# Performance work log

Hardware: AMD Instinct MI355X
Metric: run time of the kernel (lower is better)

The kernel has to match this reference:

```python
import jax, jax.numpy as jnp
import numpy as np

N_BINS = 15  # matches ECELoss(n_bins=15)


def setup_inputs() -> dict:
    key = jax.random.key(0)
    k1, k2 = jax.random.split(key)
    B, C = 2_097_152, 16
    logits = jax.random.normal(k1, (B, C), dtype=jnp.float32) * 2.0
    # binary multi-label targets, stored as float (forward casts to float anyway)
    targets = (jax.random.uniform(k2, (B, C)) < 0.5).astype(jnp.float32)
    return {"logits": logits, "targets": targets}


def reference(logits, targets):
    """Vectorized ECE: single bucketize + segment-sum pass replacing the
    per-class/per-bin Python loops. Same math: for each non-empty (class, bin)
    cell, accumulate |mean_conf - mean_acc| * (cell_count / B), then divide by
    the number of non-empty cells."""
    B, C = logits.shape
    probs = jax.nn.sigmoid(logits)  # [B, C]
    boundaries = jnp.linspace(0.0, 1.0, N_BINS + 1)
    # bin b satisfies boundaries[b] <= p < boundaries[b+1]  (>= start, < end)
    bin_idx = jnp.searchsorted(boundaries, probs, side="right") - 1  # [B, C]
    valid = (bin_idx >= 0) & (bin_idx < N_BINS)  # p == 1.0 falls in no bin
    seg = jnp.where(valid, jnp.arange(C)[None, :] * N_BINS + bin_idx, C * N_BINS)
    seg = seg.reshape(-1)
    num_seg = C * N_BINS + 1  # last segment = dumping ground for invalid
    ones = jnp.ones((B * C,), dtype=probs.dtype)
    cnt = jax.ops.segment_sum(ones, seg, num_segments=num_seg)[:-1]           # [C*n_bins]
    sum_p = jax.ops.segment_sum(probs.reshape(-1), seg, num_segments=num_seg)[:-1]
    sum_t = jax.ops.segment_sum(targets.reshape(-1), seg, num_segments=num_seg)[:-1]
    nonempty = cnt > 0
    safe = jnp.where(nonempty, cnt, 1.0)
    # |avg_confidence - accuracy| * mask.mean()  per non-empty cell
    term = jnp.abs(sum_p / safe - sum_t / safe) * (cnt / B)
    total = jnp.sum(jnp.where(nonempty, term, 0.0))
    count = jnp.sum(nonempty)
    return jnp.where(count > 0, total / count, jnp.zeros((), probs.dtype))
```

## Files before the change

### kernel.cpp

```cpp
#include <hip/hip_runtime.h>
#include <math.h>

#define NC 16
#define NBINS 15
#define NCELLS 256
#define GRID 2048
#define TPB 256
#define ITERS 64
#define STRIDE (GRID * TPB)
#define BROWS 2097152.0
#define MAXREP 8

__global__ void __launch_bounds__(256, 8) ece_partial(const float* __restrict__ logits,
                                                      const float* __restrict__ targets,
                                                      unsigned int* __restrict__ ws,
                                                      int nrep) {
    unsigned int acc[16];
#pragma unroll
    for (int k = 0; k < 16; ++k) acc[k] = 0u;

    const float LOG2E = 1.4426950408889634f;
    const int tid = blockIdx.x * TPB + threadIdx.x;

#define PROC(x, t)                                                         \
    {                                                                      \
        float e = __builtin_amdgcn_exp2f(-(x) * LOG2E);                    \
        float p = __builtin_amdgcn_rcpf(1.0f + e);                         \
        unsigned int bu = (unsigned int)(int)(p * 15.0f);       \
        unsigned int pf = (unsigned int)(p * 1024.0f + 0.5f);              \
        unsigned int val = (1u << 25) | (((unsigned int)(t)) << 18) | pf;  \
        acc[0] += val;                                                     \
        _Pragma("unroll")                                                  \
        for (int k = 1; k < 16; ++k) acc[k] += (bu >= (unsigned)k) ? val : 0u; \
    }

    for (int kk = 0; kk < ITERS; kk += 4) {
        int i0 = tid + kk * STRIDE;
        int i1 = i0 + STRIDE, i2 = i1 + STRIDE, i3 = i2 + STRIDE;
        float l0 = logits[i0], l1 = logits[i1], l2 = logits[i2], l3 = logits[i3];
        float t0 = targets[i0], t1 = targets[i1], t2 = targets[i2], t3 = targets[i3];
        PROC(l0, t0);
        PROC(l1, t1);
        PROC(l2, t2);
        PROC(l3, t3);
    }
#undef PROC

    __shared__ unsigned int h[16 * 256];
#pragma unroll
    for (int k = 0; k < 16; ++k) h[k * 256 + threadIdx.x] = acc[k];
    __syncthreads();

    int idx = threadIdx.x;
    int cls = idx & 15, lev = idx >> 4;
    int base = lev * 256 + cls;
    unsigned int cg = 0, tg = 0, pg = 0;
#pragma unroll
    for (int m = 0; m < 16; ++m) {
        unsigned int v = h[base + (((m + lev) & 15) << 4)];
        cg += v >> 25;
        tg += (v >> 18) & 127u;
        pg += v & 0x3FFFFu;
    }
    unsigned int* r = ws + (blockIdx.x & (nrep - 1)) * (3 * NCELLS);
    atomicAdd(&r[idx],              cg);
    atomicAdd(&r[NCELLS + idx],     tg);
    atomicAdd(&r[2 * NCELLS + idx], pg);
}

__global__ void __launch_bounds__(256) ece_final(const unsigned int* __restrict__ ws,
                                                 float* __restrict__ out, int nrep) {
    __shared__ unsigned int s_c[256], s_t[256], s_p[256];
    __shared__ double s_term[256];
    __shared__ int s_ne[256];
    int i = threadIdx.x;
    unsigned int cg = 0, tg = 0, pg = 0;
    for (int rep = 0; rep < nrep; ++rep) {
        const unsigned int* r = ws + rep * (3 * NCELLS);
        cg += r[i];
        tg += r[NCELLS + i];
        pg += r[2 * NCELLS + i];
    }
    s_c[i] = cg; s_t[i] = tg; s_p[i] = pg;
    __syncthreads();

    double term = 0.0;
    int ne = 0;
    int lev = i >> 4;
    if (lev < NBINS) {
        unsigned int cnt = s_c[i] - s_c[i + 16];
        if (cnt) {
            unsigned int td = s_t[i] - s_t[i + 16];
            unsigned int pd = s_p[i] - s_p[i + 16];
            double dc = (double)cnt;
            term = fabs((double)pd * (1.0 / 1024.0) / dc - (double)td / dc) *
                   (dc / BROWS);
            ne = 1;
        }
    }
    s_term[i] = term;
    s_ne[i] = ne;
    __syncthreads();
    for (int off = 128; off > 0; off >>= 1) {
        if (i < off) {
            s_term[i] += s_term[i + off];
            s_ne[i]   += s_ne[i + off];
        }
        __syncthreads();
    }
    if (i == 0) out[0] = (s_ne[0] > 0) ? (float)(s_term[0] / (double)s_ne[0]) : 0.0f;
}

extern "C" void kernel_launch(void* const* d_in, const int* in_sizes, int n_in,
                              void* d_out, int out_size, void* d_ws, size_t ws_size,
                              hipStream_t stream) {
    const float* logits  = (const float*)d_in[0];
    const float* targets = (const float*)d_in[1];
    unsigned int* ws = (unsigned int*)d_ws;
    float* out = (float*)d_out;

    int nrep = MAXREP;
    while (nrep > 1 && (size_t)(nrep * 3 * NCELLS * sizeof(unsigned int)) > ws_size)
        nrep >>= 1;

    hipMemsetAsync(ws, 0, nrep * 3 * NCELLS * sizeof(unsigned int), stream);
    ece_partial<<<GRID, TPB, 0, stream>>>(logits, targets, ws, nrep);
    ece_final<<<1, 256, 0, stream>>>(ws, out, nrep);
}
```

Baseline: 281.5 us.

## Replace per-thread cumulative bin counters with swizzled LDS atomic histogram and float4 loads

Each element used to be folded into 16 register accumulators through 15 compare-and-add steps, building a cumulative histogram. Now each element does a single LDS atomicAdd into a per-thread-column slot of a 64 KB shared histogram, swizzled to spread bank accesses. Inputs are read as float4, so each thread covers four classes, and the next pair of float4 loads is prefetched while the current pair is processed. The final kernel drops the cumulative-difference step because the histogram is now direct. The cost is a much larger LDS footprint that cuts occupancy, plus the overhead of the atomics.

```diff
diff --git a/kernel.cpp b/kernel.cpp
--- a/kernel.cpp
+++ b/kernel.cpp
@@ -1,99 +1,101 @@
 #include <hip/hip_runtime.h>
 #include <math.h>
 
-#define NC 16
 #define NBINS 15
-#define NCELLS 256
+#define NCELL (16 * NBINS)
 #define GRID 2048
 #define TPB 256
-#define ITERS 64
-#define STRIDE (GRID * TPB)
+#define ITER4 16
+#define STRIDE4 (GRID * TPB)
 #define BROWS 2097152.0
 #define MAXREP 8
 
-__global__ void __launch_bounds__(256, 8) ece_partial(const float* __restrict__ logits,
-                                                      const float* __restrict__ targets,
+__global__ void __launch_bounds__(256, 2) ece_partial(const float4* __restrict__ l4,
+                                                      const float4* __restrict__ t4,
                                                       unsigned int* __restrict__ ws,
                                                       int nrep) {
-    unsigned int acc[16];
+    __shared__ unsigned int h[256 * 64];
 #pragma unroll
-    for (int k = 0; k < 16; ++k) acc[k] = 0u;
+    for (int r = 0; r < 64; ++r) h[r * 256 + threadIdx.x] = 0u;
+    __syncthreads();
 
     const float LOG2E = 1.4426950408889634f;
-    const int tid = blockIdx.x * TPB + threadIdx.x;
+    const int tid  = blockIdx.x * TPB + threadIdx.x;
+    const int col  = threadIdx.x >> 2;
+    const int rb   = (threadIdx.x & 3) * 4 * 16;
 
-#define PROC(x, t)                                                         \
+#define PROC1(x, t, j)                                                     \
     {                                                                      \
         float e = __builtin_amdgcn_exp2f(-(x) * LOG2E);                    \
         float p = __builtin_amdgcn_rcpf(1.0f + e);                         \
-        unsigned int bu = (unsigned int)(int)(p * 15.0f);       \
-        unsigned int pf = (unsigned int)(p * 1024.0f + 0.5f);              \
-        unsigned int val = (1u << 25) | (((unsigned int)(t)) << 18) | pf;  \
-        acc[0] += val;                                                     \
-        _Pragma("unroll")                                                  \
-        for (int k = 1; k < 16; ++k) acc[k] += (bu >= (unsigned)k) ? val : 0u; \
+        int b = ((int)(p * 15.0f)) & 15;            \
+        unsigned int val = (1u << 25) | (((unsigned int)(t)) << 18) |      \
+                           (unsigned int)(p * 1024.0f + 0.5f);             \
+        int row = rb + (j) * 16 + b;                                       \
+        int addr = row * 64 + ((col + ((row >> 6) << 3)) & 63);            \
+        atomicAdd(&h[addr], val);               \
     }
+#define PROC4(lv, tv)     \
+    PROC1(lv.x, tv.x, 0); \
+    PROC1(lv.y, tv.y, 1); \
+    PROC1(lv.z, tv.z, 2); \
+    PROC1(lv.w, tv.w, 3);
 
-    for (int kk = 0; kk < ITERS; kk += 4) {
-        int i0 = tid + kk * STRIDE;
-        int i1 = i0 + STRIDE, i2 = i1 + STRIDE, i3 = i2 + STRIDE;
-        float l0 = logits[i0], l1 = logits[i1], l2 = logits[i2], l3 = logits[i3];
-        float t0 = targets[i0], t1 = targets[i1], t2 = targets[i2], t3 = targets[i3];
-        PROC(l0, t0);
-        PROC(l1, t1);
-        PROC(l2, t2);
-        PROC(l3, t3);
+    float4 c0l, c0t, c1l, c1t, n0l, n0t, n1l, n1t;
+    n0l = l4[tid];             n0t = t4[tid];
+    n1l = l4[tid + STRIDE4];   n1t = t4[tid + STRIDE4];
+
+    for (int g = 0; g < ITER4 / 2; ++g) {
+        c0l = n0l; c0t = n0t; c1l = n1l; c1t = n1t;
+        if (g < ITER4 / 2 - 1) {
+            int i0 = tid + (2 * g + 2) * STRIDE4;
+            n0l = l4[i0];           n0t = t4[i0];
+            n1l = l4[i0 + STRIDE4]; n1t = t4[i0 + STRIDE4];
+        }
+        PROC4(c0l, c0t);
+        PROC4(c1l, c1t);
     }
-#undef PROC
-
-    __shared__ unsigned int h[16 * 256];
-#pragma unroll
-    for (int k = 0; k < 16; ++k) h[k * 256 + threadIdx.x] = acc[k];
+#undef PROC4
+#undef PROC1
     __syncthreads();
 
     int idx = threadIdx.x;
-    int cls = idx & 15, lev = idx >> 4;
-    int base = lev * 256 + cls;
     unsigned int cg = 0, tg = 0, pg = 0;
 #pragma unroll
-    for (int m = 0; m < 16; ++m) {
-        unsigned int v = h[base + (((m + lev) & 15) << 4)];
+    for (int m = 0; m < 64; ++m) {
+        unsigned int v = h[idx * 64 + ((m + idx) & 63)];
         cg += v >> 25;
         tg += (v >> 18) & 127u;
         pg += v & 0x3FFFFu;
     }
-    unsigned int* r = ws + (blockIdx.x & (nrep - 1)) * (3 * NCELLS);
-    atomicAdd(&r[idx],              cg);
-    atomicAdd(&r[NCELLS + idx],     tg);
-    atomicAdd(&r[2 * NCELLS + idx], pg);
+    int bin = idx & 15, cls = idx >> 4;
+    if (bin < NBINS) {
+        int cell = cls * NBINS + bin;
+        unsigned int* r = ws + (blockIdx.x & (nrep - 1)) * (3 * NCELL);
+        atomicAdd(&r[cell],             cg);
+        atomicAdd(&r[NCELL + cell],     tg);
+        atomicAdd(&r[2 * NCELL + cell], pg);
+    }
 }
 
 __global__ void __launch_bounds__(256) ece_final(const unsigned int* __restrict__ ws,
                                                  float* __restrict__ out, int nrep) {
-    __shared__ unsigned int s_c[256], s_t[256], s_p[256];
     __shared__ double s_term[256];
     __shared__ int s_ne[256];
     int i = threadIdx.x;
-    unsigned int cg = 0, tg = 0, pg = 0;
-    for (int rep = 0; rep < nrep; ++rep) {
-        const unsigned int* r = ws + rep * (3 * NCELLS);
-        cg += r[i];
-        tg += r[NCELLS + i];
-        pg += r[2 * NCELLS + i];
-    }
-    s_c[i] = cg; s_t[i] = tg; s_p[i] = pg;
-    __syncthreads();
-
     double term = 0.0;
     int ne = 0;
-    int lev = i >> 4;
-    if (lev < NBINS) {
-        unsigned int cnt = s_c[i] - s_c[i + 16];
-        if (cnt) {
-            unsigned int td = s_t[i] - s_t[i + 16];
-            unsigned int pd = s_p[i] - s_p[i + 16];
-            double dc = (double)cnt;
-            term = fabs((double)pd * (1.0 / 1024.0) / dc - (double)td / dc) *
+    if (i < NCELL) {
+        unsigned int cg = 0, tg = 0, pg = 0;
+        for (int rep = 0; rep < nrep; ++rep) {
+            const unsigned int* r = ws + rep * (3 * NCELL);
+            cg += r[i];
+            tg += r[NCELL + i];
+            pg += r[2 * NCELL + i];
+        }
+        if (cg) {
+            double dc = (double)cg;
+            term = fabs((double)pg * (1.0 / 1024.0) / dc - (double)tg / dc) *
                    (dc / BROWS);
             ne = 1;
         }
@@ -114,16 +116,16 @@
 extern "C" void kernel_launch(void* const* d_in, const int* in_sizes, int n_in,
                               void* d_out, int out_size, void* d_ws, size_t ws_size,
                               hipStream_t stream) {
-    const float* logits  = (const float*)d_in[0];
-    const float* targets = (const float*)d_in[1];
+    const float4* logits  = (const float4*)d_in[0];
+    const float4* targets = (const float4*)d_in[1];
     unsigned int* ws = (unsigned int*)d_ws;
     float* out = (float*)d_out;
 
     int nrep = MAXREP;
-    while (nrep > 1 && (size_t)(nrep * 3 * NCELLS * sizeof(unsigned int)) > ws_size)
+    while (nrep > 1 && (size_t)(nrep * 3 * NCELL * sizeof(unsigned int)) > ws_size)
         nrep >>= 1;
 
-    hipMemsetAsync(ws, 0, nrep * 3 * NCELLS * sizeof(unsigned int), stream);
+    hipMemsetAsync(ws, 0, nrep * 3 * NCELL * sizeof(unsigned int), stream);
     ece_partial<<<GRID, TPB, 0, stream>>>(logits, targets, ws, nrep);
     ece_final<<<1, 256, 0, stream>>>(ws, out, nrep);
 }
```

New measurement: 282.7 us. Within noise of the previous version (+0.4%).
